# Kernel tuning notes

Measured on AMD Instinct MI355X. Metric: run time of the kernel, lower is better.

Reference implementation:

```python
import jax, jax.numpy as jnp
import numpy as np

N_NODES = 50000
N_EDGES = 600000
N_MOL = 512
N_ATOM_FEAT = 30   # NUMBER_ATOMIC_GRAPH_FEATURES
N_BOND_FEAT = 10   # NUMBER_BOND_GRAPH_FEATURES


def _sh(v):
    # Real solid spherical harmonics l=0..3, e3nn 'component' normalization
    # (sum_m Y_lm^2 = (2l+1) r^{2l}), normalize=False -> homogeneous polynomials.
    x, y, z = v[..., 0], v[..., 1], v[..., 2]
    r2 = x * x + y * y + z * z
    s3, s5, s15, s105 = 3 ** 0.5, 5 ** 0.5, 15 ** 0.5, 105 ** 0.5
    s70_4, s42_4, s7_2, s105_2 = 70 ** 0.5 / 4, 42 ** 0.5 / 4, 7 ** 0.5 / 2, 105 ** 0.5 / 2
    return jnp.stack([
        jnp.ones_like(x),                                               # l=0
        s3 * x, s3 * y, s3 * z,                                         # l=1
        s15 * x * y, s15 * y * z, 0.5 * s5 * (3 * z * z - r2),
        s15 * x * z, 0.5 * s15 * (x * x - y * y),                       # l=2
        s70_4 * y * (3 * x * x - y * y), s105 * x * y * z,
        s42_4 * y * (5 * z * z - r2), s7_2 * z * (5 * z * z - 3 * r2),
        s42_4 * x * (5 * z * z - r2), s105_2 * z * (x * x - y * y),
        s70_4 * x * (x * x - 3 * y * y),                                # l=3 (no TP path uses it)
    ], axis=-1)


def setup_inputs() -> dict:
    key = jax.random.key(0)
    ks = jax.random.split(key, 12)
    positions = jax.random.normal(ks[0], (N_NODES, 3), jnp.float32)
    x = jax.random.normal(ks[1], (N_NODES, N_ATOM_FEAT), jnp.float32)
    edge_attr = jax.random.normal(ks[2], (N_EDGES, N_BOND_FEAT), jnp.float32)
    edge_src = jax.random.randint(ks[3], (N_EDGES,), 0, N_NODES)
    edge_dst = jax.random.randint(ks[4], (N_EDGES,), 0, N_NODES)
    batch = jnp.sort(jax.random.randint(ks[5], (N_NODES,), 0, N_MOL))
    # tp1: FullyConnectedTensorProduct(30x0e, sh) -> live outputs 64x0e + 24x1o + 16x2e
    W1_0 = jax.random.normal(ks[6], (N_ATOM_FEAT, 64), jnp.float32)
    W1_1 = jax.random.normal(ks[7], (N_ATOM_FEAT, 24), jnp.float32)
    W1_2 = jax.random.normal(ks[8], (N_ATOM_FEAT, 16), jnp.float32)
    # tp2: paths 0e*0e, 1o*1o, 2e*2e -> 1x0e
    W2_0 = jax.random.normal(ks[9], (64,), jnp.float32)
    W2_1 = jax.random.normal(ks[10], (24,), jnp.float32)
    W2_2 = jax.random.normal(ks[11], (16,), jnp.float32)
    return dict(positions=positions, x=x, edge_attr=edge_attr,
                W1_0=W1_0, W1_1=W1_1, W1_2=W1_2,
                W2_0=W2_0, W2_1=W2_1, W2_2=W2_2,
                edge_src=edge_src, edge_dst=edge_dst, batch=batch)


def _forward(positions, x, edge_attr, W1_0, W1_1, W1_2, W2_0, W2_1, W2_2,
             edge_src, edge_dst, batch):
    E = edge_src.shape[0]
    seg = jax.ops.segment_sum
    edge_vec = positions[edge_src] - positions[edge_dst]            # [E,3]
    sh = _sh(edge_vec)                                              # [E,16]
    # mul_edges TP: only bond channel 0 has instructions; path_weight sqrt(2l+1)
    # cancels w3j(0,l,l)=I/sqrt(2l+1) exactly -> plain product.
    ea = edge_attr[:, :1] * sh
    ea0, ea1, ea2 = ea[:, 0:1], ea[:, 1:4], ea[:, 4:9]              # l=3 slice unused (no path)
    deg = seg(jnp.ones((E,), sh.dtype), edge_dst, num_segments=N_NODES)
    inv_sqrt_deg = jnp.where(deg > 0, jax.lax.rsqrt(jnp.maximum(deg, 1.0)), 0.0)[:, None]
    # tp1: 0e x l -> l ; path_weight*w3j collapses to 1/sqrt(fan_in=30)
    W1 = jnp.concatenate([W1_0, W1_1, W1_2], axis=1)                # [30,104]
    a = (x[edge_src] @ W1) * (1.0 / np.sqrt(N_ATOM_FEAT))           # [E,104]
    a0, a1, a2 = a[:, :64], a[:, 64:88], a[:, 88:104]
    e_feat = jnp.concatenate([
        a0 * ea0,                                                   # [E,64]  0e
        (a1[:, :, None] * ea1[:, None, :]).reshape(E, 72),          # [E,24*3] 1o
        (a2[:, :, None] * ea2[:, None, :]).reshape(E, 80),          # [E,16*5] 2e
    ], axis=1)                                                      # [E,216]
    n = seg(e_feat, edge_dst, num_segments=N_NODES) * inv_sqrt_deg  # [N,216]
    # tp2: l x l -> 0e, w3j(l,l,0)=I/sqrt(2l+1), path_weight = 1/sqrt(104)
    g = n[edge_src]                                                 # [E,216]
    t0 = (g[:, :64] * ea0) @ W2_0
    t1 = jnp.einsum('eum,em,u->e', g[:, 64:136].reshape(E, 24, 3), ea1, W2_1)
    t2 = jnp.einsum('eum,em,u->e', g[:, 136:216].reshape(E, 16, 5), ea2, W2_2)
    out_e = (t0 + t1 / np.sqrt(3.0) + t2 / np.sqrt(5.0)) * (1.0 / np.sqrt(104.0))
    node = seg(out_e[:, None], edge_dst, num_segments=N_NODES) * inv_sqrt_deg  # [N,1]
    acc = seg(node, batch, num_segments=N_MOL)                      # [M,1]
    atoms = seg(jnp.ones((N_NODES,), node.dtype), batch, num_segments=N_MOL)[:, None]
    return acc * jnp.where(atoms > 0, jax.lax.rsqrt(jnp.maximum(atoms, 1.0)), 0.0)


def reference(positions, x, edge_attr, W1_0, W1_1, W1_2, W2_0, W2_1, W2_2,
              edge_src, edge_dst, batch):
    return _forward(positions, x, edge_attr, W1_0, W1_1, W1_2,
                    W2_0, W2_1, W2_2, edge_src, edge_dst, batch)
```

## Files before the change

### kernel.cpp

```cpp
#include <hip/hip_runtime.h>

#define DEV_INLINE __device__ __forceinline__

static DEV_INLINE void sh_l012(float xx, float yy, float zz, float sh[9]) {
    const float s3  = 1.7320508075688772f;
    const float s5  = 2.23606797749979f;
    const float s15 = 3.872983346207417f;
    float r2 = xx * xx + yy * yy + zz * zz;
    sh[0] = 1.0f;
    sh[1] = s3 * xx;
    sh[2] = s3 * yy;
    sh[3] = s3 * zz;
    sh[4] = s15 * xx * yy;
    sh[5] = s15 * yy * zz;
    sh[6] = 0.5f * s5 * (3.0f * zz * zz - r2);
    sh[7] = s15 * xx * zz;
    sh[8] = 0.5f * s15 * (xx * xx - yy * yy);
}

__global__ void k_prep(const float* __restrict__ x,
                       const float* __restrict__ pos,
                       const float* __restrict__ W1_0, const float* __restrict__ W1_1,
                       const float* __restrict__ W1_2, const float* __restrict__ W2_0,
                       const float* __restrict__ W2_1, const float* __restrict__ W2_2,
                       const int* __restrict__ edst,
                       float4* __restrict__ node1, float2* __restrict__ node2,
                       int* __restrict__ deg, int n_nodes, int n_edges) {
    __shared__ float ws[90];
    int t = threadIdx.x;
    int g = blockIdx.x * blockDim.x + t;
    bool nodeBlock = (blockIdx.x * blockDim.x) < n_nodes;
    if (nodeBlock) {
        const float inv_s30 = 0.18257418583505536f;
        if (t < 30) {
            float s = 0.f;
            for (int u = 0; u < 64; u++) s += W1_0[t * 64 + u] * W2_0[u];
            ws[t] = s * inv_s30;
        } else if (t < 60) {
            int k = t - 30;
            float s = 0.f;
            for (int u = 0; u < 24; u++) s += W1_1[k * 24 + u] * W2_1[u];
            ws[t] = s * inv_s30;
        } else if (t < 90) {
            int k = t - 60;
            float s = 0.f;
            for (int u = 0; u < 16; u++) s += W1_2[k * 16 + u] * W2_2[u];
            ws[t] = s * inv_s30;
        }
        __syncthreads();
        if (g < n_nodes) {
            const float* xv = x + (size_t)g * 30;
            float s0 = 0.f, s1 = 0.f, s2 = 0.f;
#pragma unroll
            for (int k = 0; k < 30; k++) {
                float xk = xv[k];
                s0 += xk * ws[k];
                s1 += xk * ws[30 + k];
                s2 += xk * ws[60 + k];
            }
            node1[g] = make_float4(pos[g * 3 + 0], pos[g * 3 + 1], pos[g * 3 + 2], s0);
            node2[g] = make_float2(s1, s2);
        }
    }
    int e0 = 2 * g, e1 = 2 * g + 1;
    if (e1 < n_edges) {
        int2 d2 = ((const int2*)edst)[g];
        atomicAdd(deg + d2.x, 1);
        atomicAdd(deg + d2.y, 1);
    } else if (e0 < n_edges) {
        atomicAdd(deg + edst[e0], 1);
    }
}

__global__ void k_scan1(const int* __restrict__ deg, int* __restrict__ blocksum, int n_nodes) {
    __shared__ int s[256];
    int t = threadIdx.x;
    int v = blockIdx.x * 256 + t;
    s[t] = (v < n_nodes) ? deg[v] : 0;
    __syncthreads();
    for (int off = 128; off > 0; off >>= 1) {
        if (t < off) s[t] += s[t + off];
        __syncthreads();
    }
    if (t == 0) blocksum[blockIdx.x] = s[0];
}

__global__ void k_scan2(const int* __restrict__ blocksum, int* __restrict__ blockoff, int nb) {
    __shared__ int s[256];
    int t = threadIdx.x;
    int val = (t < nb) ? blocksum[t] : 0;
    s[t] = val;
    __syncthreads();
    for (int off = 1; off < 256; off <<= 1) {
        int y = (t >= off) ? s[t - off] : 0;
        __syncthreads();
        s[t] += y;
        __syncthreads();
    }
    if (t < nb) blockoff[t] = s[t] - val;
}

__global__ void k_scan3(const int* __restrict__ deg, const int* __restrict__ blockoff,
                        int* __restrict__ rowptr, const int* __restrict__ batch,
                        int* __restrict__ atoms, int n_nodes) {
    __shared__ int s[256];
    __shared__ int hist[512];
    int t = threadIdx.x;
    int v = blockIdx.x * 256 + t;
    int val = (v < n_nodes) ? deg[v] : 0;
    s[t] = val;
    hist[t] = 0;
    hist[t + 256] = 0;
    __syncthreads();
    for (int off = 1; off < 256; off <<= 1) {
        int y = (t >= off) ? s[t - off] : 0;
        __syncthreads();
        s[t] += y;
        __syncthreads();
    }
    if (v < n_nodes) rowptr[v] = blockoff[blockIdx.x] + s[t] - val;
    int v0 = blockIdx.x * 256;
    if (v0 < n_nodes) {
        int molFirst = batch[v0];
        int vend = min(v0 + 255, n_nodes - 1);
        int molLast = batch[vend];
        if (v < n_nodes) atomicAdd(&hist[batch[v] - molFirst], 1);
        __syncthreads();
        for (int m = t; m <= molLast - molFirst; m += 256)
            if (hist[m] > 0) atomicAdd(atoms + molFirst + m, hist[m]);
    }
}

__global__ void k_place(const float* __restrict__ eattr, const int* __restrict__ esrc,
                        const int* __restrict__ edst, const int* __restrict__ rowptr,
                        int* __restrict__ cursor, int2* __restrict__ rec, int n_edges) {
    int g = blockIdx.x * blockDim.x + threadIdx.x;
    int e0 = 2 * g, e1 = 2 * g + 1;
    if (e1 < n_edges) {
        int2 d2 = ((const int2*)edst)[g];
        int2 s2 = ((const int2*)esrc)[g];
        float ea0 = eattr[(size_t)e0 * 10];
        float ea1 = eattr[(size_t)e1 * 10];
        int slot0 = rowptr[d2.x] + atomicAdd(cursor + d2.x, 1);
        int slot1 = rowptr[d2.y] + atomicAdd(cursor + d2.y, 1);
        rec[slot0] = make_int2(s2.x, __float_as_int(ea0));
        rec[slot1] = make_int2(s2.y, __float_as_int(ea1));
    } else if (e0 < n_edges) {
        int dst = edst[e0];
        int slot = rowptr[dst] + atomicAdd(cursor + dst, 1);
        rec[slot] = make_int2(esrc[e0], __float_as_int(eattr[(size_t)e0 * 10]));
    }
}

__global__ void k_passA(const float4* __restrict__ node1, const float2* __restrict__ node2,
                        const int2* __restrict__ rec,
                        const int* __restrict__ rowptr, const int* __restrict__ deg,
                        float4* __restrict__ Pkg, int n_nodes) {
    int g = blockIdx.x * blockDim.x + threadIdx.x;
    int v = g >> 3, r = g & 7;
    if (v >= n_nodes) return;
    int beg = rowptr[v], d = deg[v];
    float4 pv = node1[v];
    float acc[9];
#pragma unroll
    for (int m = 0; m < 9; m++) acc[m] = 0.f;
    for (int i = beg + r; i < beg + d; i += 8) {
        int2 rcd = rec[i];
        int src = rcd.x;
        float ea = __int_as_float(rcd.y);
        float4 n1 = node1[src];
        float2 n2 = node2[src];
        float dx = n1.x - pv.x, dy = n1.y - pv.y, dz = n1.z - pv.z;
        float sh[9];
        sh_l012(dx, dy, dz, sh);
        acc[0] += ea * n1.w;
#pragma unroll
        for (int m = 1; m < 4; m++) acc[m] += ea * sh[m] * n2.x;
#pragma unroll
        for (int m = 4; m < 9; m++) acc[m] += ea * sh[m] * n2.y;
    }
#pragma unroll
    for (int off = 1; off < 8; off <<= 1)
#pragma unroll
        for (int m = 0; m < 9; m++) acc[m] += __shfl_xor(acc[m], off);
    if (r == 0) {
        float s = (d > 0) ? rsqrtf((float)d) : 0.f;
        float4* out = Pkg + (size_t)v * 3;
        out[0] = make_float4(acc[0] * s, acc[1] * s, acc[2] * s, acc[3] * s);
        out[1] = make_float4(acc[4] * s, acc[5] * s, acc[6] * s, acc[7] * s);
        out[2] = make_float4(acc[8] * s, pv.x, pv.y, pv.z);
    }
}

__global__ void k_passB(const float4* __restrict__ node1, const float4* __restrict__ Pkg,
                        const int2* __restrict__ rec,
                        const int* __restrict__ rowptr, const int* __restrict__ deg,
                        const int* __restrict__ batch,
                        float* __restrict__ accmol, int n_nodes) {
    __shared__ float smol[512];
    int t = threadIdx.x;
    smol[t] = 0.f;
    smol[t + 256] = 0.f;
    __syncthreads();
    int g = blockIdx.x * blockDim.x + t;
    int v = g >> 3, r = g & 7;
    int v0 = (blockIdx.x * blockDim.x) >> 3;
    const float i3 = 0.5773502691896258f;
    const float i5 = 0.4472135954999579f;
    const float i104 = 0.09805806756909202f;
    int molFirst = batch[min(v0, n_nodes - 1)];
    if (v < n_nodes) {
        int beg = rowptr[v], d = deg[v];
        float4 pv = node1[v];
        float s = 0.f;
        for (int i = beg + r; i < beg + d; i += 8) {
            int2 rcd = rec[i];
            int src = rcd.x;
            float ea = __int_as_float(rcd.y);
            const float4* Ps = Pkg + (size_t)src * 3;
            float4 p03 = Ps[0];
            float4 p47 = Ps[1];
            float4 p8p = Ps[2];
            float dx = p8p.y - pv.x, dy = p8p.z - pv.y, dz = p8p.w - pv.z;
            float sh[9];
            sh_l012(dx, dy, dz, sh);
            float t1 = sh[1] * p03.y + sh[2] * p03.z + sh[3] * p03.w;
            float t2 = sh[4] * p47.x + sh[5] * p47.y + sh[6] * p47.z + sh[7] * p47.w + sh[8] * p8p.x;
            s += ea * (p03.x + t1 * i3 + t2 * i5);
        }
#pragma unroll
        for (int off = 1; off < 8; off <<= 1) s += __shfl_xor(s, off);
        if (r == 0) {
            float isd = (d > 0) ? rsqrtf((float)d) : 0.f;
            atomicAdd(&smol[batch[v] - molFirst], s * i104 * isd);
        }
    }
    __syncthreads();
    if (v0 < n_nodes) {
        int vend = min(v0 + 31, n_nodes - 1);
        int nm = batch[vend] - molFirst + 1;
        for (int m = t; m < nm; m += 256) {
            float val = smol[m];
            if (val != 0.f) atomicAdd(accmol + molFirst + m, val);
        }
    }
}

__global__ void k_final(const float* __restrict__ acc, const int* __restrict__ atoms,
                        float* __restrict__ out, int n_mol) {
    int m = blockIdx.x * blockDim.x + threadIdx.x;
    if (m >= n_mol) return;
    int a = atoms[m];
    out[m] = (a > 0) ? acc[m] * rsqrtf((float)a) : 0.f;
}

extern "C" void kernel_launch(void* const* d_in, const int* in_sizes, int n_in,
                              void* d_out, int out_size, void* d_ws, size_t ws_size,
                              hipStream_t stream) {
    const float* pos   = (const float*)d_in[0];
    const float* x     = (const float*)d_in[1];
    const float* eattr = (const float*)d_in[2];
    const float* W1_0  = (const float*)d_in[3];
    const float* W1_1  = (const float*)d_in[4];
    const float* W1_2  = (const float*)d_in[5];
    const float* W2_0  = (const float*)d_in[6];
    const float* W2_1  = (const float*)d_in[7];
    const float* W2_2  = (const float*)d_in[8];
    const int* esrc  = (const int*)d_in[9];
    const int* edst  = (const int*)d_in[10];
    const int* batch = (const int*)d_in[11];

    const int n_edges = in_sizes[9];
    const int n_nodes = in_sizes[11];
    const int n_mol   = out_size;
    float* out = (float*)d_out;

    const int BS = 256;
    const int NB = (n_nodes + BS - 1) / BS;
    const int EB2 = (n_edges / 2 + BS - 1) / BS;
    const int VB8 = (8 * n_nodes + BS - 1) / BS;

    char* ws = (char*)d_ws;
    size_t off = 0;
    auto carve = [&](size_t bytes) {
        size_t o = off;
        off = (off + bytes + 255) & ~(size_t)255;
        return o;
    };
    size_t off_deg    = carve((size_t)n_nodes * sizeof(int));
    size_t off_cur    = carve((size_t)n_nodes * sizeof(int));
    size_t off_acc    = carve((size_t)n_mol * sizeof(float));
    size_t off_atoms  = carve((size_t)n_mol * sizeof(int));
    size_t zero_bytes = off;
    size_t off_rowptr = carve((size_t)n_nodes * sizeof(int));
    size_t off_bsum   = carve((size_t)NB * sizeof(int));
    size_t off_boff   = carve((size_t)NB * sizeof(int));
    size_t off_n1     = carve((size_t)n_nodes * sizeof(float4));
    size_t off_n2     = carve((size_t)n_nodes * sizeof(float2));
    size_t off_Pkg    = carve((size_t)n_nodes * 3 * sizeof(float4));
    size_t off_rec    = carve((size_t)n_edges * sizeof(int2));
    (void)ws_size;

    int*    deg    = (int*)(ws + off_deg);
    int*    cursor = (int*)(ws + off_cur);
    float*  accmol = (float*)(ws + off_acc);
    int*    atoms  = (int*)(ws + off_atoms);
    int*    rowptr = (int*)(ws + off_rowptr);
    int*    bsum   = (int*)(ws + off_bsum);
    int*    boff   = (int*)(ws + off_boff);
    float4* node1  = (float4*)(ws + off_n1);
    float2* node2  = (float2*)(ws + off_n2);
    float4* Pkg    = (float4*)(ws + off_Pkg);
    int2*   rec    = (int2*)(ws + off_rec);

    hipMemsetAsync(d_ws, 0, zero_bytes, stream);

    k_prep<<<EB2, BS, 0, stream>>>(x, pos, W1_0, W1_1, W1_2, W2_0, W2_1, W2_2,
                                   edst, node1, node2, deg, n_nodes, n_edges);
    k_scan1<<<NB, BS, 0, stream>>>(deg, bsum, n_nodes);
    k_scan2<<<1, 256, 0, stream>>>(bsum, boff, NB);
    k_scan3<<<NB, BS, 0, stream>>>(deg, boff, rowptr, batch, atoms, n_nodes);
    k_place<<<EB2, BS, 0, stream>>>(eattr, esrc, edst, rowptr, cursor, rec, n_edges);
    k_passA<<<VB8, BS, 0, stream>>>(node1, node2, rec, rowptr, deg, Pkg, n_nodes);
    k_passB<<<VB8, BS, 0, stream>>>(node1, Pkg, rec, rowptr, deg, batch, accmol, n_nodes);
    k_final<<<(n_mol + BS - 1) / BS, BS, 0, stream>>>(accmol, atoms, out, n_mol);
}
```

Measured before the change: 181.5 us.

## Fuse scan kernels via last-block pattern, record atomic ranks, widen per-node lanes

The degree-counting pass now keeps each edge's atomic return value as its rank within its destination row and compacts the first edge attribute into a dense array. The placement kernel then needs no second round of atomics on a cursor array. The three scan kernels become one: a last-block-done counter finishes the block-offset scan, and consumers add the block offset to the local row pointer. PassA and passB use 16 lanes per node instead of 8. This cuts two launches and one atomic pass, at the cost of extra rank and attribute arrays and more idle lanes on low-degree nodes.

```diff
diff --git a/kernel.cpp b/kernel.cpp
--- a/kernel.cpp
+++ b/kernel.cpp
@@ -23,9 +23,10 @@
                        const float* __restrict__ W1_0, const float* __restrict__ W1_1,
                        const float* __restrict__ W1_2, const float* __restrict__ W2_0,
                        const float* __restrict__ W2_1, const float* __restrict__ W2_2,
-                       const int* __restrict__ edst,
+                       const int* __restrict__ edst, const float* __restrict__ eattr,
                        float4* __restrict__ node1, float2* __restrict__ node2,
-                       int* __restrict__ deg, int n_nodes, int n_edges) {
+                       int* __restrict__ deg, int* __restrict__ rank, float* __restrict__ eac,
+                       int n_nodes, int n_edges) {
     __shared__ float ws[90];
     int t = threadIdx.x;
     int g = blockIdx.x * blockDim.x + t;
@@ -65,46 +66,26 @@
     int e0 = 2 * g, e1 = 2 * g + 1;
     if (e1 < n_edges) {
         int2 d2 = ((const int2*)edst)[g];
-        atomicAdd(deg + d2.x, 1);
-        atomicAdd(deg + d2.y, 1);
+        float ea0 = eattr[(size_t)e0 * 10];
+        float ea1 = eattr[(size_t)e1 * 10];
+        int r0 = atomicAdd(deg + d2.x, 1);
+        int r1 = atomicAdd(deg + d2.y, 1);
+        ((int2*)rank)[g] = make_int2(r0, r1);
+        ((float2*)eac)[g] = make_float2(ea0, ea1);
     } else if (e0 < n_edges) {
-        atomicAdd(deg + edst[e0], 1);
-    }
-}
-
-__global__ void k_scan1(const int* __restrict__ deg, int* __restrict__ blocksum, int n_nodes) {
-    __shared__ int s[256];
-    int t = threadIdx.x;
-    int v = blockIdx.x * 256 + t;
-    s[t] = (v < n_nodes) ? deg[v] : 0;
-    __syncthreads();
-    for (int off = 128; off > 0; off >>= 1) {
-        if (t < off) s[t] += s[t + off];
-        __syncthreads();
-    }
-    if (t == 0) blocksum[blockIdx.x] = s[0];
-}
-
-__global__ void k_scan2(const int* __restrict__ blocksum, int* __restrict__ blockoff, int nb) {
-    __shared__ int s[256];
-    int t = threadIdx.x;
-    int val = (t < nb) ? blocksum[t] : 0;
-    s[t] = val;
-    __syncthreads();
-    for (int off = 1; off < 256; off <<= 1) {
-        int y = (t >= off) ? s[t - off] : 0;
-        __syncthreads();
-        s[t] += y;
-        __syncthreads();
-    }
-    if (t < nb) blockoff[t] = s[t] - val;
-}
-
-__global__ void k_scan3(const int* __restrict__ deg, const int* __restrict__ blockoff,
-                        int* __restrict__ rowptr, const int* __restrict__ batch,
-                        int* __restrict__ atoms, int n_nodes) {
+        float ea0 = eattr[(size_t)e0 * 10];
+        rank[e0] = atomicAdd(deg + edst[e0], 1);
+        eac[e0] = ea0;
+    }
+}
+
+__global__ void k_scan(const int* __restrict__ deg, const int* __restrict__ batch,
+                       int* __restrict__ rowptr_local, int* __restrict__ bsum,
+                       int* __restrict__ blockoff, int* __restrict__ atoms,
+                       int* __restrict__ done, int n_nodes) {
     __shared__ int s[256];
     __shared__ int hist[512];
+    __shared__ int lastFlag;
     int t = threadIdx.x;
     int v = blockIdx.x * 256 + t;
     int val = (v < n_nodes) ? deg[v] : 0;
@@ -118,53 +99,73 @@
         s[t] += y;
         __syncthreads();
     }
-    if (v < n_nodes) rowptr[v] = blockoff[blockIdx.x] + s[t] - val;
+    if (v < n_nodes) rowptr_local[v] = s[t] - val;
+    if (t == 255) bsum[blockIdx.x] = s[255];
     int v0 = blockIdx.x * 256;
-    if (v0 < n_nodes) {
-        int molFirst = batch[v0];
-        int vend = min(v0 + 255, n_nodes - 1);
-        int molLast = batch[vend];
-        if (v < n_nodes) atomicAdd(&hist[batch[v] - molFirst], 1);
+    int molFirst = batch[min(v0, n_nodes - 1)];
+    if (v < n_nodes) atomicAdd(&hist[batch[v] - molFirst], 1);
+    __syncthreads();
+    int vend = min(v0 + 255, n_nodes - 1);
+    int molLast = batch[vend];
+    for (int m = t; m <= molLast - molFirst; m += 256)
+        if (hist[m] > 0) atomicAdd(atoms + molFirst + m, hist[m]);
+    if (t == 0) {
+        __threadfence();
+        lastFlag = (atomicAdd(done, 1) == gridDim.x - 1) ? 1 : 0;
+    }
+    __syncthreads();
+    if (lastFlag) {
+        int nb = gridDim.x;
+        int bv = (t < nb) ? bsum[t] : 0;
+        s[t] = bv;
         __syncthreads();
-        for (int m = t; m <= molLast - molFirst; m += 256)
-            if (hist[m] > 0) atomicAdd(atoms + molFirst + m, hist[m]);
-    }
-}
-
-__global__ void k_place(const float* __restrict__ eattr, const int* __restrict__ esrc,
-                        const int* __restrict__ edst, const int* __restrict__ rowptr,
-                        int* __restrict__ cursor, int2* __restrict__ rec, int n_edges) {
+        for (int off = 1; off < 256; off <<= 1) {
+            int y = (t >= off) ? s[t - off] : 0;
+            __syncthreads();
+            s[t] += y;
+            __syncthreads();
+        }
+        if (t < nb) blockoff[t] = s[t] - bv;
+    }
+}
+
+__global__ void k_place(const int* __restrict__ esrc, const int* __restrict__ edst,
+                        const int* __restrict__ rank, const float* __restrict__ eac,
+                        const int* __restrict__ rowptr_local, const int* __restrict__ blockoff,
+                        int2* __restrict__ rec, int n_edges) {
     int g = blockIdx.x * blockDim.x + threadIdx.x;
     int e0 = 2 * g, e1 = 2 * g + 1;
     if (e1 < n_edges) {
         int2 d2 = ((const int2*)edst)[g];
         int2 s2 = ((const int2*)esrc)[g];
-        float ea0 = eattr[(size_t)e0 * 10];
-        float ea1 = eattr[(size_t)e1 * 10];
-        int slot0 = rowptr[d2.x] + atomicAdd(cursor + d2.x, 1);
-        int slot1 = rowptr[d2.y] + atomicAdd(cursor + d2.y, 1);
-        rec[slot0] = make_int2(s2.x, __float_as_int(ea0));
-        rec[slot1] = make_int2(s2.y, __float_as_int(ea1));
+        int2 r2 = ((const int2*)rank)[g];
+        float2 ea2 = ((const float2*)eac)[g];
+        int slot0 = rowptr_local[d2.x] + blockoff[d2.x >> 8] + r2.x;
+        int slot1 = rowptr_local[d2.y] + blockoff[d2.y >> 8] + r2.y;
+        rec[slot0] = make_int2(s2.x, __float_as_int(ea2.x));
+        rec[slot1] = make_int2(s2.y, __float_as_int(ea2.y));
     } else if (e0 < n_edges) {
         int dst = edst[e0];
-        int slot = rowptr[dst] + atomicAdd(cursor + dst, 1);
-        rec[slot] = make_int2(esrc[e0], __float_as_int(eattr[(size_t)e0 * 10]));
+        int slot = rowptr_local[dst] + blockoff[dst >> 8] + rank[e0];
+        rec[slot] = make_int2(esrc[e0], __float_as_int(eac[e0]));
     }
 }
 
 __global__ void k_passA(const float4* __restrict__ node1, const float2* __restrict__ node2,
                         const int2* __restrict__ rec,
-                        const int* __restrict__ rowptr, const int* __restrict__ deg,
+                        const int* __restrict__ rowptr_local, const int* __restrict__ blockoff,
+                        const int* __restrict__ deg,
                         float4* __restrict__ Pkg, int n_nodes) {
     int g = blockIdx.x * blockDim.x + threadIdx.x;
-    int v = g >> 3, r = g & 7;
+    int v = g >> 4, r = g & 15;
     if (v >= n_nodes) return;
-    int beg = rowptr[v], d = deg[v];
+    int beg = rowptr_local[v] + blockoff[v >> 8];
+    int d = deg[v];
     float4 pv = node1[v];
     float acc[9];
 #pragma unroll
     for (int m = 0; m < 9; m++) acc[m] = 0.f;
-    for (int i = beg + r; i < beg + d; i += 8) {
+    for (int i = beg + r; i < beg + d; i += 16) {
         int2 rcd = rec[i];
         int src = rcd.x;
         float ea = __int_as_float(rcd.y);
@@ -180,7 +181,7 @@
         for (int m = 4; m < 9; m++) acc[m] += ea * sh[m] * n2.y;
     }
 #pragma unroll
-    for (int off = 1; off < 8; off <<= 1)
+    for (int off = 1; off < 16; off <<= 1)
 #pragma unroll
         for (int m = 0; m < 9; m++) acc[m] += __shfl_xor(acc[m], off);
     if (r == 0) {
@@ -194,8 +195,8 @@
 
 __global__ void k_passB(const float4* __restrict__ node1, const float4* __restrict__ Pkg,
                         const int2* __restrict__ rec,
-                        const int* __restrict__ rowptr, const int* __restrict__ deg,
-                        const int* __restrict__ batch,
+                        const int* __restrict__ rowptr_local, const int* __restrict__ blockoff,
+                        const int* __restrict__ deg, const int* __restrict__ batch,
                         float* __restrict__ accmol, int n_nodes) {
     __shared__ float smol[512];
     int t = threadIdx.x;
@@ -203,17 +204,18 @@
     smol[t + 256] = 0.f;
     __syncthreads();
     int g = blockIdx.x * blockDim.x + t;
-    int v = g >> 3, r = g & 7;
-    int v0 = (blockIdx.x * blockDim.x) >> 3;
+    int v = g >> 4, r = g & 15;
+    int v0 = blockIdx.x * 16;
     const float i3 = 0.5773502691896258f;
     const float i5 = 0.4472135954999579f;
     const float i104 = 0.09805806756909202f;
     int molFirst = batch[min(v0, n_nodes - 1)];
     if (v < n_nodes) {
-        int beg = rowptr[v], d = deg[v];
+        int beg = rowptr_local[v] + blockoff[v >> 8];
+        int d = deg[v];
         float4 pv = node1[v];
         float s = 0.f;
-        for (int i = beg + r; i < beg + d; i += 8) {
+        for (int i = beg + r; i < beg + d; i += 16) {
             int2 rcd = rec[i];
             int src = rcd.x;
             float ea = __int_as_float(rcd.y);
@@ -229,7 +231,7 @@
             s += ea * (p03.x + t1 * i3 + t2 * i5);
         }
 #pragma unroll
-        for (int off = 1; off < 8; off <<= 1) s += __shfl_xor(s, off);
+        for (int off = 1; off < 16; off <<= 1) s += __shfl_xor(s, off);
         if (r == 0) {
             float isd = (d > 0) ? rsqrtf((float)d) : 0.f;
             atomicAdd(&smol[batch[v] - molFirst], s * i104 * isd);
@@ -237,7 +239,7 @@
     }
     __syncthreads();
     if (v0 < n_nodes) {
-        int vend = min(v0 + 31, n_nodes - 1);
+        int vend = min(v0 + 15, n_nodes - 1);
         int nm = batch[vend] - molFirst + 1;
         for (int m = t; m < nm; m += 256) {
             float val = smol[m];
@@ -278,7 +280,7 @@
     const int BS = 256;
     const int NB = (n_nodes + BS - 1) / BS;
     const int EB2 = (n_edges / 2 + BS - 1) / BS;
-    const int VB8 = (8 * n_nodes + BS - 1) / BS;
+    const int VB16 = (16 * n_nodes + BS - 1) / BS;
 
     char* ws = (char*)d_ws;
     size_t off = 0;
@@ -288,40 +290,43 @@
         return o;
     };
     size_t off_deg    = carve((size_t)n_nodes * sizeof(int));
-    size_t off_cur    = carve((size_t)n_nodes * sizeof(int));
     size_t off_acc    = carve((size_t)n_mol * sizeof(float));
     size_t off_atoms  = carve((size_t)n_mol * sizeof(int));
+    size_t off_done   = carve(sizeof(int));
     size_t zero_bytes = off;
-    size_t off_rowptr = carve((size_t)n_nodes * sizeof(int));
+    size_t off_rpl    = carve((size_t)n_nodes * sizeof(int));
     size_t off_bsum   = carve((size_t)NB * sizeof(int));
     size_t off_boff   = carve((size_t)NB * sizeof(int));
     size_t off_n1     = carve((size_t)n_nodes * sizeof(float4));
     size_t off_n2     = carve((size_t)n_nodes * sizeof(float2));
     size_t off_Pkg    = carve((size_t)n_nodes * 3 * sizeof(float4));
     size_t off_rec    = carve((size_t)n_edges * sizeof(int2));
+    size_t off_rank   = carve((size_t)n_edges * sizeof(int));
+    size_t off_eac    = carve((size_t)n_edges * sizeof(float));
     (void)ws_size;
 
     int*    deg    = (int*)(ws + off_deg);
-    int*    cursor = (int*)(ws + off_cur);
     float*  accmol = (float*)(ws + off_acc);
     int*    atoms  = (int*)(ws + off_atoms);
-    int*    rowptr = (int*)(ws + off_rowptr);
+    int*    done   = (int*)(ws + off_done);
+    int*    rpl    = (int*)(ws + off_rpl);
     int*    bsum   = (int*)(ws + off_bsum);
     int*    boff   = (int*)(ws + off_boff);
     float4* node1  = (float4*)(ws + off_n1);
     float2* node2  = (float2*)(ws + off_n2);
     float4* Pkg    = (float4*)(ws + off_Pkg);
     int2*   rec    = (int2*)(ws + off_rec);
+    int*    rank   = (int*)(ws + off_rank);
+    float*  eac    = (float*)(ws + off_eac);
 
     hipMemsetAsync(d_ws, 0, zero_bytes, stream);
 
     k_prep<<<EB2, BS, 0, stream>>>(x, pos, W1_0, W1_1, W1_2, W2_0, W2_1, W2_2,
-                                   edst, node1, node2, deg, n_nodes, n_edges);
-    k_scan1<<<NB, BS, 0, stream>>>(deg, bsum, n_nodes);
-    k_scan2<<<1, 256, 0, stream>>>(bsum, boff, NB);
-    k_scan3<<<NB, BS, 0, stream>>>(deg, boff, rowptr, batch, atoms, n_nodes);
-    k_place<<<EB2, BS, 0, stream>>>(eattr, esrc, edst, rowptr, cursor, rec, n_edges);
-    k_passA<<<VB8, BS, 0, stream>>>(node1, node2, rec, rowptr, deg, Pkg, n_nodes);
-    k_passB<<<VB8, BS, 0, stream>>>(node1, Pkg, rec, rowptr, deg, batch, accmol, n_nodes);
+                                   edst, eattr, node1, node2, deg, rank, eac,
+                                   n_nodes, n_edges);
+    k_scan<<<NB, BS, 0, stream>>>(deg, batch, rpl, bsum, boff, atoms, done, n_nodes);
+    k_place<<<EB2, BS, 0, stream>>>(esrc, edst, rank, eac, rpl, boff, rec, n_edges);
+    k_passA<<<VB16, BS, 0, stream>>>(node1, node2, rec, rpl, boff, deg, Pkg, n_nodes);
+    k_passB<<<VB16, BS, 0, stream>>>(node1, Pkg, rec, rpl, boff, deg, batch, accmol, n_nodes);
     k_final<<<(n_mol + BS - 1) / BS, BS, 0, stream>>>(accmol, atoms, out, n_mol);
 }
```

Measured after the change: 162.0 us. 10.7% less time.
